# Kernel tuning notes

Measured on AMD Instinct MI355X. Metric: run time of the kernel, lower is better.

## Reference

```python
import jax, jax.numpy as jnp
import numpy as np

O, I, B = 4096, 4096, 4096  # out_features, in_features, flattened tokens
GROUP = 128
INIT_PEAK = 2.0


def setup_inputs() -> dict:
    key = jax.random.key(0)
    k1, k2, k3, k4 = jax.random.split(key, 4)
    x = jax.random.normal(k1, (B, I), jnp.float32)
    # initial_ternary in {-1,0,1} -> theta init per the torch constructor
    tern = jax.random.randint(k2, (O, I), -1, 2)
    theta_neg = jnp.where(tern == -1, INIT_PEAK, -INIT_PEAK).astype(jnp.float32)
    theta_pos = jnp.where(tern == 1, INIT_PEAK, -INIT_PEAK).astype(jnp.float32)
    # per-group scales expanded to full weight shape (scales.unsqueeze(1).expand.reshape)
    n_groups = O * I // GROUP
    scales = jax.random.uniform(k3, (n_groups,), jnp.float32, 0.01, 0.05)
    scales_exp = jnp.repeat(scales, GROUP).reshape(O, I)
    # reparameterization noise (training path), made explicit for determinism
    eps = jax.random.normal(k4, (B, O), jnp.float32)
    return {"x": x, "theta_neg": theta_neg, "theta_pos": theta_pos,
            "scales_exp": scales_exp, "eps": eps}


def reference(x, theta_neg, theta_pos, scales_exp, eps):
    # stable 3-way softmax over logits [theta_neg, 0, theta_pos], done without
    # materializing the stacked [O, I, 3] tensor
    m = jnp.maximum(jnp.maximum(theta_neg, theta_pos), 0.0)
    e_neg = jnp.exp(theta_neg - m)
    e_zero = jnp.exp(-m)
    e_pos = jnp.exp(theta_pos - m)
    Z = e_neg + e_zero + e_pos
    p_neg = e_neg / Z
    p_pos = e_pos / Z
    diff = p_pos - p_neg
    w_mean = diff * scales_exp                                   # [O, I]
    w_var = (p_pos + p_neg - diff * diff) * (scales_exp * scales_exp)  # [O, I]
    mu = x @ w_mean.T                                            # [B, O]
    sigma_sq = (x * x) @ w_var.T                                 # [B, O]
    sigma = jnp.sqrt(jnp.maximum(sigma_sq, 1e-8))
    return mu + sigma * eps
```

## Files before the change

### kernel.cpp

```cpp
#include <hip/hip_runtime.h>

#define I_DIM 4096
#define O_DIM 4096
#define B_DIM 4096

typedef _Float16 f16;
typedef __attribute__((ext_vector_type(4))) _Float16 f16x4;
typedef __attribute__((ext_vector_type(8))) _Float16 f16x8;
typedef __attribute__((ext_vector_type(4))) float f32x4;

struct f16pair { f16 m, v; };

__device__ inline f16pair lr_wmv(float tn, float tp, float s) {
    float m = fmaxf(fmaxf(tn, tp), 0.0f);
    float en = __expf(tn - m);
    float ez = __expf(-m);
    float ep = __expf(tp - m);
    float inv = __builtin_amdgcn_rcpf(en + ez + ep);
    float pn = en * inv, pp = ep * inv;
    float d = pp - pn;
    f16pair r;
    r.m = (f16)(d * s);
    r.v = (f16)((pp + pn - d * d) * (s * s));
    return r;
}

__global__ __launch_bounds__(256)
void prep_all(const float4* __restrict__ x, f16x4* __restrict__ xb4,
              const float4* __restrict__ tn4, const float4* __restrict__ tp4,
              const float4* __restrict__ sc4,
              f16x4* __restrict__ wm4, f16x4* __restrict__ wv4) {
    const int G = (int)((size_t)O_DIM * I_DIM / 4);
    const int nt = gridDim.x * blockDim.x;
    const int t0 = blockIdx.x * blockDim.x + threadIdx.x;

    for (int g = t0; g < G; g += nt) {
        float4 a = x[g];
        f16x4 o;
        o[0] = (f16)a.x; o[1] = (f16)a.y; o[2] = (f16)a.z; o[3] = (f16)a.w;
        xb4[g] = o;
    }
    for (int g = t0; g < G; g += nt) {
        float4 a = tn4[g], b = tp4[g], s = sc4[g];
        f16x4 om, ov;
        f16pair p;
        p = lr_wmv(a.x, b.x, s.x); om[0] = p.m; ov[0] = p.v;
        p = lr_wmv(a.y, b.y, s.y); om[1] = p.m; ov[1] = p.v;
        p = lr_wmv(a.z, b.z, s.z); om[2] = p.m; ov[2] = p.v;
        p = lr_wmv(a.w, b.w, s.w); om[3] = p.m; ov[3] = p.v;
        wm4[g] = om;
        wv4[g] = ov;
    }
}

#define BM 256
#define BN 128
#define BK 64

__device__ inline void gl_lds16(const f16* g, f16* l) {
    __builtin_amdgcn_global_load_lds(
        (const __attribute__((address_space(1))) unsigned int*)g,
        (__attribute__((address_space(3))) unsigned int*)l,
        16, 0, 0);
}

#define VM8 asm volatile("s_waitcnt vmcnt(8)")
#define VM6 asm volatile("s_waitcnt vmcnt(6)")
#define VM4 asm volatile("s_waitcnt vmcnt(4)")
#define VM0 asm volatile("s_waitcnt vmcnt(0)")
#define VMNONE (void)0

__global__ __launch_bounds__(512, 2)
void fused_dual_gemm(const f16* __restrict__ Xb,
                     const f16* __restrict__ Wm, const f16* __restrict__ Wv,
                     const float* __restrict__ eps, float* __restrict__ out) {
    __shared__ f16 smem[65536];

    const int tid  = threadIdx.x;
    const int lane = tid & 63;
    const int wave = tid >> 6;

    const int bm = blockIdx.y * BM;
    const int bn = blockIdx.x * BN;

    const int srow = lane >> 2;
    const int scol = (((lane & 3) ^ ((lane >> 3) & 3)) << 3);
    const f16* gX = Xb + (size_t)(bm + 32 * wave + srow) * I_DIM + scol;
    const f16* gM = Wm + (size_t)(bn + 16 * wave + srow) * I_DIM + scol;
    const f16* gV = Wv + (size_t)(bn + 16 * wave + srow) * I_DIM + scol;
    f16* ldsX = smem + wave * 1024;
    f16* ldsW = smem + 16384 + wave * 512;

    const int fr  = lane & 15;
    const int sg8 = (((lane >> 4) ^ ((fr >> 1) & 3)) << 3);
    const int m0 = (wave >> 1) << 6;
    const int n0 = (wave & 1) << 6;

    f32x4 accM[4][4];
    f32x4 accV[4][4];
    const f32x4 z = {0.0f, 0.0f, 0.0f, 0.0f};
#pragma unroll
    for (int mi = 0; mi < 4; ++mi)
#pragma unroll
        for (int ni = 0; ni < 4; ++ni) { accM[mi][ni] = z; accV[mi][ni] = z; }

    f16x8 A0[4], A1[4], A2c[4], Ba[4], Bb[4];

#define STAGE_X(kelem, reg) do {                                               \
        gl_lds16(gX + (kelem),              ldsX + (reg));                     \
        gl_lds16(gX + (kelem) + 16 * I_DIM, ldsX + (reg) + 512);               \
    } while (0)
#define STAGE_W(kelem, reg) do {                                               \
        gl_lds16(gM + (kelem), ldsW + (reg));                                  \
        gl_lds16(gV + (kelem), ldsW + (reg) + 4096);                           \
    } while (0)

#define RD_A(DST, RX) do {                                                     \
        DST[0] = *(const f16x8*)(smem + (RX) + (m0 +  0 + fr) * 32 + sg8);     \
        DST[1] = *(const f16x8*)(smem + (RX) + (m0 + 16 + fr) * 32 + sg8);     \
        DST[2] = *(const f16x8*)(smem + (RX) + (m0 + 32 + fr) * 32 + sg8);     \
        DST[3] = *(const f16x8*)(smem + (RX) + (m0 + 48 + fr) * 32 + sg8);     \
    } while (0)
#define RD_B(DST, RW, H) do {                                                  \
        DST[0] = *(const f16x8*)(smem + (RW)        + (n0 + (H)*32 +  0 + fr) * 32 + sg8); \
        DST[1] = *(const f16x8*)(smem + (RW) + 4096 + (n0 + (H)*32 +  0 + fr) * 32 + sg8); \
        DST[2] = *(const f16x8*)(smem + (RW)        + (n0 + (H)*32 + 16 + fr) * 32 + sg8); \
        DST[3] = *(const f16x8*)(smem + (RW) + 4096 + (n0 + (H)*32 + 16 + fr) * 32 + sg8); \
    } while (0)

#define MFMA8(AC, BB, NI0, NI1, MI0, MI1) do {                                 \
        accM[MI0][NI0] = __builtin_amdgcn_mfma_f32_16x16x32_f16(AC[MI0],  BB[0], accM[MI0][NI0], 0, 0, 0); \
        accV[MI0][NI0] = __builtin_amdgcn_mfma_f32_16x16x32_f16(A2c[MI0], BB[1], accV[MI0][NI0], 0, 0, 0); \
        accM[MI0][NI1] = __builtin_amdgcn_mfma_f32_16x16x32_f16(AC[MI0],  BB[2], accM[MI0][NI1], 0, 0, 0); \
        accV[MI0][NI1] = __builtin_amdgcn_mfma_f32_16x16x32_f16(A2c[MI0], BB[3], accV[MI0][NI1], 0, 0, 0); \
        accM[MI1][NI0] = __builtin_amdgcn_mfma_f32_16x16x32_f16(AC[MI1],  BB[0], accM[MI1][NI0], 0, 0, 0); \
        accV[MI1][NI0] = __builtin_amdgcn_mfma_f32_16x16x32_f16(A2c[MI1], BB[1], accV[MI1][NI0], 0, 0, 0); \
        accM[MI1][NI1] = __builtin_amdgcn_mfma_f32_16x16x32_f16(AC[MI1],  BB[2], accM[MI1][NI1], 0, 0, 0); \
        accV[MI1][NI1] = __builtin_amdgcn_mfma_f32_16x16x32_f16(A2c[MI1], BB[3], accV[MI1][NI1], 0, 0, 0); \
    } while (0)

#define A2C(AC) do {                                                           \
        _Pragma("unroll")                                                      \
        for (int mi = 0; mi < 4; ++mi) A2c[mi] = AC[mi] * AC[mi];              \
    } while (0)

#define PH_EVEN(AC, RWcur, STG, VM) do {                                       \
        STG;                                                                   \
        A2C(AC);                                                               \
        __builtin_amdgcn_s_setprio(1);                                         \
        MFMA8(AC, Ba, 0, 1, 0, 1);                                             \
        RD_B(Bb, RWcur, 1);                                                    \
        MFMA8(AC, Ba, 0, 1, 2, 3);                                             \
        __builtin_amdgcn_s_setprio(0);                                         \
        VM; __builtin_amdgcn_s_barrier();                                      \
    } while (0)
#define PH_ODD(AC, ANext, RXn, RWn, STG, VM) do {                              \
        STG;                                                                   \
        __builtin_amdgcn_s_setprio(1);                                         \
        MFMA8(AC, Bb, 2, 3, 0, 1);                                             \
        RD_A(ANext, RXn);                                                      \
        MFMA8(AC, Bb, 2, 3, 2, 3);                                             \
        __builtin_amdgcn_s_setprio(0);                                         \
        RD_B(Ba, RWn, 0);                                                      \
        VM; __builtin_amdgcn_s_barrier();                                      \
    } while (0)

    STAGE_X(0, 0);      STAGE_W(0, 0);
    STAGE_X(32, 8192);  STAGE_W(32, 8192);
    STAGE_X(64, 32768); STAGE_W(64, 32768);
    VM8;
    __builtin_amdgcn_s_barrier();
    RD_A(A0, 0);
    RD_B(Ba, 16384, 0);

#pragma unroll 1
    for (int i = 0; i < 31; ++i) {
        const int kb = i * 128;
        PH_EVEN(A0, 16384,            STAGE_X(kb +  96, 40960), VM6);
        PH_ODD (A0, A1, 8192, 24576,  STAGE_W(kb +  96, 40960), VMNONE);
        PH_EVEN(A1, 24576,            STAGE_X(kb + 128,     0), VM6);
        PH_ODD (A1, A0, 32768, 49152, STAGE_W(kb + 128,     0), VMNONE);
        PH_EVEN(A0, 49152,            STAGE_X(kb + 160,  8192), VM6);
        PH_ODD (A0, A1, 40960, 57344, STAGE_W(kb + 160,  8192), VMNONE);
        PH_EVEN(A1, 57344,            STAGE_X(kb + 192, 32768), VM6);
        PH_ODD (A1, A0, 0, 16384,     STAGE_W(kb + 192, 32768), VMNONE);
    }

    PH_EVEN(A0, 16384,            STAGE_X(4064, 40960), VM6);
    PH_ODD (A0, A1, 8192, 24576,  STAGE_W(4064, 40960), VMNONE);
    PH_EVEN(A1, 24576,            VMNONE, VM4);
    PH_ODD (A1, A0, 32768, 49152, VMNONE, VMNONE);
    PH_EVEN(A0, 49152,            VMNONE, VM0);
    PH_ODD (A0, A1, 40960, 57344, VMNONE, VMNONE);
    PH_EVEN(A1, 57344,            VMNONE, VMNONE);
    MFMA8(A1, Bb, 2, 3, 0, 1);
    MFMA8(A1, Bb, 2, 3, 2, 3);

    const int oc  = lane & 15;
    const int orb = (lane >> 4) << 2;
#pragma unroll
    for (int mi = 0; mi < 4; ++mi) {
#pragma unroll
        for (int ni = 0; ni < 4; ++ni) {
            const int gn = bn + n0 + ni * 16 + oc;
            const int gm = bm + m0 + mi * 16 + orb;
#pragma unroll
            for (int r = 0; r < 4; ++r) {
                const size_t off = (size_t)(gm + r) * O_DIM + gn;
                const float mu = accM[mi][ni][r];
                const float vv = accV[mi][ni][r];
                out[off] = fmaf(sqrtf(fmaxf(vv, 1e-8f)), eps[off], mu);
            }
        }
    }
#undef PH_ODD
#undef PH_EVEN
#undef A2C
#undef MFMA8
#undef RD_B
#undef RD_A
#undef STAGE_W
#undef STAGE_X
}

extern "C" void kernel_launch(void* const* d_in, const int* in_sizes, int n_in,
                              void* d_out, int out_size, void* d_ws, size_t ws_size,
                              hipStream_t stream) {
    const float* x   = (const float*)d_in[0];
    const float* tn  = (const float*)d_in[1];
    const float* tp  = (const float*)d_in[2];
    const float* sc  = (const float*)d_in[3];
    const float* eps = (const float*)d_in[4];
    float* out = (float*)d_out;

    const size_t NE = (size_t)O_DIM * I_DIM;
    f16* xb = (f16*)d_ws;
    f16* wm = xb + NE;
    f16* wv = wm + NE;

    prep_all<<<2048, 256, 0, stream>>>(
        (const float4*)x, (f16x4*)xb,
        (const float4*)tn, (const float4*)tp, (const float4*)sc,
        (f16x4*)wm, (f16x4*)wv);

    dim3 grid(O_DIM / BN, B_DIM / BM);
    fused_dual_gemm<<<grid, 512, 0, stream>>>(
        (const f16*)xb, (const f16*)wm, (const f16*)wv, eps, out);
}
```

Measured before the change: 544.0 us.

## Switch dual GEMM from 16x16x32 to 32x32x16 MFMA tiles

Replaces the 16x16x32 f16 MFMA instructions with 32x32x16 ones. Each wave now holds 2x2 accumulator tiles of 16 floats instead of 4x4 tiles of 4 floats. The LDS fragment reads and swizzle offsets are recomputed for the 32-row layout, and the epilogue store mapping is rewritten to match. The goal is to issue fewer MFMA instructions and cut LDS read traffic per FLOP through larger tiles, in exchange for a different output store pattern and dependency latency.

Result: slower. 1.014 ms (+86.3%).

```diff
diff --git a/kernel.cpp b/kernel.cpp
--- a/kernel.cpp
+++ b/kernel.cpp
@@ -8,6 +8,7 @@
 typedef __attribute__((ext_vector_type(4))) _Float16 f16x4;
 typedef __attribute__((ext_vector_type(8))) _Float16 f16x8;
 typedef __attribute__((ext_vector_type(4))) float f32x4;
+typedef __attribute__((ext_vector_type(16))) float f32x16;
 
 struct f16pair { f16 m, v; };
 
@@ -70,6 +71,8 @@
 #define VM0 asm volatile("s_waitcnt vmcnt(0)")
 #define VMNONE (void)0
 
+#define MFMA32(A_, B_, C_) __builtin_amdgcn_mfma_f32_32x32x16_f16((A_), (B_), (C_), 0, 0, 0)
+
 __global__ __launch_bounds__(512, 2)
 void fused_dual_gemm(const f16* __restrict__ Xb,
                      const f16* __restrict__ Wm, const f16* __restrict__ Wv,
@@ -91,18 +94,21 @@
     f16* ldsX = smem + wave * 1024;
     f16* ldsW = smem + 16384 + wave * 512;
 
-    const int fr  = lane & 15;
-    const int sg8 = (((lane >> 4) ^ ((fr >> 1) & 3)) << 3);
+    const int r5 = lane & 31;
+    const int hi = lane >> 5;
+    const int e0 = ((hi ^ ((r5 >> 1) & 3)) << 3);
     const int m0 = (wave >> 1) << 6;
     const int n0 = (wave & 1) << 6;
 
-    f32x4 accM[4][4];
-    f32x4 accV[4][4];
-    const f32x4 z = {0.0f, 0.0f, 0.0f, 0.0f};
-#pragma unroll
-    for (int mi = 0; mi < 4; ++mi)
-#pragma unroll
-        for (int ni = 0; ni < 4; ++ni) { accM[mi][ni] = z; accV[mi][ni] = z; }
+    f32x16 accM[2][2];
+    f32x16 accV[2][2];
+#pragma unroll
+    for (int mi = 0; mi < 2; ++mi)
+#pragma unroll
+        for (int ni = 0; ni < 2; ++ni) {
+#pragma unroll
+            for (int j = 0; j < 16; ++j) { accM[mi][ni][j] = 0.0f; accV[mi][ni][j] = 0.0f; }
+        }
 
     f16x8 A0[4], A1[4], A2c[4], Ba[4], Bb[4];
 
@@ -115,53 +121,55 @@
         gl_lds16(gV + (kelem), ldsW + (reg) + 4096);                           \
     } while (0)
 
-#define RD_A(DST, RX) do {                                                     \
-        DST[0] = *(const f16x8*)(smem + (RX) + (m0 +  0 + fr) * 32 + sg8);     \
-        DST[1] = *(const f16x8*)(smem + (RX) + (m0 + 16 + fr) * 32 + sg8);     \
-        DST[2] = *(const f16x8*)(smem + (RX) + (m0 + 32 + fr) * 32 + sg8);     \
-        DST[3] = *(const f16x8*)(smem + (RX) + (m0 + 48 + fr) * 32 + sg8);     \
-    } while (0)
-#define RD_B(DST, RW, H) do {                                                  \
-        DST[0] = *(const f16x8*)(smem + (RW)        + (n0 + (H)*32 +  0 + fr) * 32 + sg8); \
-        DST[1] = *(const f16x8*)(smem + (RW) + 4096 + (n0 + (H)*32 +  0 + fr) * 32 + sg8); \
-        DST[2] = *(const f16x8*)(smem + (RW)        + (n0 + (H)*32 + 16 + fr) * 32 + sg8); \
-        DST[3] = *(const f16x8*)(smem + (RW) + 4096 + (n0 + (H)*32 + 16 + fr) * 32 + sg8); \
-    } while (0)
-
-#define MFMA8(AC, BB, NI0, NI1, MI0, MI1) do {                                 \
-        accM[MI0][NI0] = __builtin_amdgcn_mfma_f32_16x16x32_f16(AC[MI0],  BB[0], accM[MI0][NI0], 0, 0, 0); \
-        accV[MI0][NI0] = __builtin_amdgcn_mfma_f32_16x16x32_f16(A2c[MI0], BB[1], accV[MI0][NI0], 0, 0, 0); \
-        accM[MI0][NI1] = __builtin_amdgcn_mfma_f32_16x16x32_f16(AC[MI0],  BB[2], accM[MI0][NI1], 0, 0, 0); \
-        accV[MI0][NI1] = __builtin_amdgcn_mfma_f32_16x16x32_f16(A2c[MI0], BB[3], accV[MI0][NI1], 0, 0, 0); \
-        accM[MI1][NI0] = __builtin_amdgcn_mfma_f32_16x16x32_f16(AC[MI1],  BB[0], accM[MI1][NI0], 0, 0, 0); \
-        accV[MI1][NI0] = __builtin_amdgcn_mfma_f32_16x16x32_f16(A2c[MI1], BB[1], accV[MI1][NI0], 0, 0, 0); \
-        accM[MI1][NI1] = __builtin_amdgcn_mfma_f32_16x16x32_f16(AC[MI1],  BB[2], accM[MI1][NI1], 0, 0, 0); \
-        accV[MI1][NI1] = __builtin_amdgcn_mfma_f32_16x16x32_f16(A2c[MI1], BB[3], accV[MI1][NI1], 0, 0, 0); \
+#define RD_A32(DST, RX) do {                                                   \
+        DST[0] = *(const f16x8*)(smem + (RX) + (m0 +  0 + r5) * 32 + e0);      \
+        DST[1] = *(const f16x8*)(smem + (RX) + (m0 +  0 + r5) * 32 + (e0 ^ 16)); \
+        DST[2] = *(const f16x8*)(smem + (RX) + (m0 + 32 + r5) * 32 + e0);      \
+        DST[3] = *(const f16x8*)(smem + (RX) + (m0 + 32 + r5) * 32 + (e0 ^ 16)); \
+    } while (0)
+#define RD_B32(DST, RW, NI) do {                                               \
+        DST[0] = *(const f16x8*)(smem + (RW)        + (n0 + (NI)*32 + r5) * 32 + e0); \
+        DST[1] = *(const f16x8*)(smem + (RW) + 4096 + (n0 + (NI)*32 + r5) * 32 + e0); \
+        DST[2] = *(const f16x8*)(smem + (RW)        + (n0 + (NI)*32 + r5) * 32 + (e0 ^ 16)); \
+        DST[3] = *(const f16x8*)(smem + (RW) + 4096 + (n0 + (NI)*32 + r5) * 32 + (e0 ^ 16)); \
+    } while (0)
+
+#define MFMA4a(AC, BB, NI) do {                                                \
+        accM[0][NI] = MFMA32(AC[0],  BB[0], accM[0][NI]);                      \
+        accV[0][NI] = MFMA32(A2c[0], BB[1], accV[0][NI]);                      \
+        accM[1][NI] = MFMA32(AC[2],  BB[0], accM[1][NI]);                      \
+        accV[1][NI] = MFMA32(A2c[2], BB[1], accV[1][NI]);                      \
+    } while (0)
+#define MFMA4b(AC, BB, NI) do {                                                \
+        accM[0][NI] = MFMA32(AC[1],  BB[2], accM[0][NI]);                      \
+        accV[0][NI] = MFMA32(A2c[1], BB[3], accV[0][NI]);                      \
+        accM[1][NI] = MFMA32(AC[3],  BB[2], accM[1][NI]);                      \
+        accV[1][NI] = MFMA32(A2c[3], BB[3], accV[1][NI]);                      \
     } while (0)
 
 #define A2C(AC) do {                                                           \
         _Pragma("unroll")                                                      \
-        for (int mi = 0; mi < 4; ++mi) A2c[mi] = AC[mi] * AC[mi];              \
+        for (int j = 0; j < 4; ++j) A2c[j] = AC[j] * AC[j];                    \
     } while (0)
 
 #define PH_EVEN(AC, RWcur, STG, VM) do {                                       \
         STG;                                                                   \
         A2C(AC);                                                               \
         __builtin_amdgcn_s_setprio(1);                                         \
-        MFMA8(AC, Ba, 0, 1, 0, 1);                                             \
-        RD_B(Bb, RWcur, 1);                                                    \
-        MFMA8(AC, Ba, 0, 1, 2, 3);                                             \
+        MFMA4a(AC, Ba, 0);                                                     \
+        RD_B32(Bb, RWcur, 1);                                                  \
+        MFMA4b(AC, Ba, 0);                                                     \
         __builtin_amdgcn_s_setprio(0);                                         \
         VM; __builtin_amdgcn_s_barrier();                                      \
     } while (0)
 #define PH_ODD(AC, ANext, RXn, RWn, STG, VM) do {                              \
         STG;                                                                   \
         __builtin_amdgcn_s_setprio(1);                                         \
-        MFMA8(AC, Bb, 2, 3, 0, 1);                                             \
-        RD_A(ANext, RXn);                                                      \
-        MFMA8(AC, Bb, 2, 3, 2, 3);                                             \
+        MFMA4a(AC, Bb, 1);                                                     \
+        RD_A32(ANext, RXn);                                                    \
+        MFMA4b(AC, Bb, 1);                                                     \
         __builtin_amdgcn_s_setprio(0);                                         \
-        RD_B(Ba, RWn, 0);                                                      \
+        RD_B32(Ba, RWn, 0);                                                    \
         VM; __builtin_amdgcn_s_barrier();                                      \
     } while (0)
 
@@ -170,8 +178,8 @@
     STAGE_X(64, 32768); STAGE_W(64, 32768);
     VM8;
     __builtin_amdgcn_s_barrier();
-    RD_A(A0, 0);
-    RD_B(Ba, 16384, 0);
+    RD_A32(A0, 0);
+    RD_B32(Ba, 16384, 0);
 
 #pragma unroll 1
     for (int i = 0; i < 31; ++i) {
@@ -193,32 +201,35 @@
     PH_EVEN(A0, 49152,            VMNONE, VM0);
     PH_ODD (A0, A1, 40960, 57344, VMNONE, VMNONE);
     PH_EVEN(A1, 57344,            VMNONE, VMNONE);
-    MFMA8(A1, Bb, 2, 3, 0, 1);
-    MFMA8(A1, Bb, 2, 3, 2, 3);
-
-    const int oc  = lane & 15;
-    const int orb = (lane >> 4) << 2;
-#pragma unroll
-    for (int mi = 0; mi < 4; ++mi) {
-#pragma unroll
-        for (int ni = 0; ni < 4; ++ni) {
-            const int gn = bn + n0 + ni * 16 + oc;
-            const int gm = bm + m0 + mi * 16 + orb;
-#pragma unroll
-            for (int r = 0; r < 4; ++r) {
-                const size_t off = (size_t)(gm + r) * O_DIM + gn;
-                const float mu = accM[mi][ni][r];
-                const float vv = accV[mi][ni][r];
-                out[off] = fmaf(sqrtf(fmaxf(vv, 1e-8f)), eps[off], mu);
+    MFMA4a(A1, Bb, 1);
+    MFMA4b(A1, Bb, 1);
+
+#pragma unroll
+    for (int mi = 0; mi < 2; ++mi) {
+#pragma unroll
+        for (int ni = 0; ni < 2; ++ni) {
+            const int gn  = bn + n0 + ni * 32 + r5;
+            const int gmb = bm + m0 + mi * 32 + 4 * hi;
+#pragma unroll
+            for (int q = 0; q < 4; ++q) {
+#pragma unroll
+                for (int r = 0; r < 4; ++r) {
+                    const int row = gmb + q * 8 + r;
+                    const size_t off = (size_t)row * O_DIM + gn;
+                    const float mu = accM[mi][ni][q * 4 + r];
+                    const float vv = accV[mi][ni][q * 4 + r];
+                    out[off] = fmaf(sqrtf(fmaxf(vv, 1e-8f)), eps[off], mu);
+                }
             }
         }
     }
 #undef PH_ODD
 #undef PH_EVEN
 #undef A2C
-#undef MFMA8
-#undef RD_B
-#undef RD_A
+#undef MFMA4a
+#undef MFMA4b
+#undef RD_B32
+#undef RD_A32
 #undef STAGE_W
 #undef STAGE_X
 }
```
